# Performance work log

Measured on AMD Instinct MI355X. Metric: run time of the kernel, lower is better.

## Reference

```python
import jax, jax.numpy as jnp
import numpy as np

# ---- constants derived from init_kwargs ----
DETECT_THRESHOLD = 3.0
DETECT_SIGN = -1          # negative spikes
MARGIN_LEFT = 20          # snippet_T1
MARGIN_RIGHT = 20         # snippet_T2
CHANNEL_RADIUS = 100.0
SAMPLING_FREQUENCY = 30000.0
TIME_RADIUS = int(np.ceil(0.5 / 1000.0 * SAMPLING_FREQUENCY))  # = 15
MAX_DETECTIONS = 100000   # static cap for jit-compatible compaction


def setup_inputs() -> dict:
    key = jax.random.key(0)
    k1, k2 = jax.random.split(key)
    traces = jax.random.normal(k1, (150000, 384), dtype=jnp.float32)
    # spread channels over a 2000x2000 um area so radius=100 gives sparse adjacency
    channel_locations = jax.random.uniform(k2, (384, 2), dtype=jnp.float32) * 2000.0
    return {"traces": traces, "channel_locations": channel_locations}


def _detect_mask(traces, channel_locations):
    N, M = traces.shape
    # orientation (detect_sign < 0 -> traces_inv = -traces)
    if DETECT_SIGN > 0:
        traces_inv = traces
    elif DETECT_SIGN == 0:
        traces_inv = jnp.abs(traces)
    else:
        traces_inv = -traces

    # temporal max-pool, kernel 2*TR+1, stride 1, same padding (pads with -inf)
    pool = 2 * TIME_RADIUS + 1
    neg_inf = jnp.float32(-jnp.inf)
    temporal_max = jax.lax.reduce_window(
        traces_inv, neg_inf, jax.lax.max,
        window_dimensions=(pool, 1), window_strides=(1, 1),
        padding=((TIME_RADIUS, TIME_RADIUS), (0, 0)))  # [N, M]

    # channel adjacency from pairwise distances
    diff = channel_locations[:, None, :] - channel_locations[None, :, :]
    dists = jnp.sqrt(jnp.sum(diff * diff, axis=-1))  # [M, M]
    adj = dists <= CHANNEL_RADIUS

    # per-channel masked neighbor max over temporal_max columns -> [N, M]
    # sequential lax.map over channels avoids an N x M x M intermediate
    spatial_max = jax.lax.map(
        lambda row: jnp.max(jnp.where(row[None, :], temporal_max, neg_inf), axis=1),
        adj).T  # [N, M]

    t = jnp.arange(N)
    margin_ok = (t >= MARGIN_LEFT) & (t < N - MARGIN_RIGHT)  # [N]

    valid = ((traces_inv == temporal_max)
             & (traces_inv >= DETECT_THRESHOLD)
             & margin_ok[:, None]
             & (traces_inv >= spatial_max))
    return valid, traces_inv


def reference(traces, channel_locations):
    valid, _ = _detect_mask(traces, channel_locations)
    # row-major nonzero order == stable sort by time (row index)
    times, chans = jnp.nonzero(valid, size=MAX_DETECTIONS, fill_value=-1)
    return times.astype(jnp.int64), chans.astype(jnp.int32)
```

## Files before the change

### kernel.cpp

```cpp
#include <hip/hip_runtime.h>
#include <stdint.h>

#define M_CH       384
#define TR         15
#define MARGIN     20
#define CHUNK_ROWS 16
#define BM_WORDS   192
#define WPR        12
#define WIN_ROWS   46

__device__ __forceinline__ uint32_t spread4(uint32_t x) {
    x = (x | (x << 12)) & 0x000F000Fu;
    x = (x | (x << 6))  & 0x03030303u;
    x = (x | (x << 3))  & 0x11111111u;
    return x;
}

__global__ __launch_bounds__(256)
void cand_kernel(const float* __restrict__ traces,
                 const float* __restrict__ locs,
                 long n4, long nwords, int nbrBlock,
                 uint32_t* __restrict__ candWords,
                 uint32_t* __restrict__ nEntries,
                 uint8_t* __restrict__ entryWord,
                 uint32_t* __restrict__ entryMask) {
    if ((int)blockIdx.x >= nbrBlock) {
        __shared__ float lx[M_CH], ly[M_CH];
        const int t = threadIdx.x;
        for (int c = t; c < M_CH; c += 256) {
            lx[c] = locs[2 * c];
            ly[c] = locs[2 * c + 1];
        }
        __syncthreads();
        for (int c0 = t; c0 < M_CH; c0 += 256) {
            float x = lx[c0], y = ly[c0];
            int ne = 0;
            for (int k = 0; k < WPR; ++k) {
                uint32_t mk = 0;
                #pragma unroll
                for (int b = 0; b < 32; ++b) {
                    int c = k * 32 + b;
                    float dx = x - lx[c], dy = y - ly[c];
                    if (sqrtf(dx * dx + dy * dy) <= 100.0f) mk |= 1u << b;
                }
                if (mk) {
                    entryWord[c0 * WPR + ne] = (uint8_t)k;
                    entryMask[c0 * WPR + ne] = mk;
                    ne++;
                }
            }
            nEntries[c0] = (uint32_t)ne;
        }
        return;
    }

    const int lane = threadIdx.x & 63;
    const long wv = (((long)blockIdx.x * 256) + threadIdx.x) >> 6;
    const long fb = wv * 256;
    uint64_t B00,B01,B02,B03, B10,B11,B12,B13,
             B20,B21,B22,B23, B30,B31,B32,B33;
    {
        float4 v0 = make_float4(0,0,0,0), v1 = v0, v2 = v0, v3 = v0;
        long i0 = fb + 0 * 64 + lane;
        long i1 = fb + 1 * 64 + lane;
        long i2 = fb + 2 * 64 + lane;
        long i3 = fb + 3 * 64 + lane;
        if (i0 < n4) v0 = ((const float4*)traces)[i0];
        if (i1 < n4) v1 = ((const float4*)traces)[i1];
        if (i2 < n4) v2 = ((const float4*)traces)[i2];
        if (i3 < n4) v3 = ((const float4*)traces)[i3];
        B00 = __ballot(v0.x <= -3.0f); B01 = __ballot(v0.y <= -3.0f);
        B02 = __ballot(v0.z <= -3.0f); B03 = __ballot(v0.w <= -3.0f);
        B10 = __ballot(v1.x <= -3.0f); B11 = __ballot(v1.y <= -3.0f);
        B12 = __ballot(v1.z <= -3.0f); B13 = __ballot(v1.w <= -3.0f);
        B20 = __ballot(v2.x <= -3.0f); B21 = __ballot(v2.y <= -3.0f);
        B22 = __ballot(v2.z <= -3.0f); B23 = __ballot(v2.w <= -3.0f);
        B30 = __ballot(v3.x <= -3.0f); B31 = __ballot(v3.y <= -3.0f);
        B32 = __ballot(v3.z <= -3.0f); B33 = __ballot(v3.w <= -3.0f);
    }
    if (lane < 32) {
        int k  = lane >> 3;
        int sh = (lane & 7) * 8;
        uint64_t b0 = (k & 2) ? ((k & 1) ? B30 : B20) : ((k & 1) ? B10 : B00);
        uint64_t b1 = (k & 2) ? ((k & 1) ? B31 : B21) : ((k & 1) ? B11 : B01);
        uint64_t b2 = (k & 2) ? ((k & 1) ? B32 : B22) : ((k & 1) ? B12 : B02);
        uint64_t b3 = (k & 2) ? ((k & 1) ? B33 : B23) : ((k & 1) ? B13 : B03);
        uint32_t w = spread4((uint32_t)(b0 >> sh) & 0xFFu)
                   | (spread4((uint32_t)(b1 >> sh) & 0xFFu) << 1)
                   | (spread4((uint32_t)(b2 >> sh) & 0xFFu) << 2)
                   | (spread4((uint32_t)(b3 >> sh) & 0xFFu) << 3);
        long wIdx = wv * 32 + lane;
        if (wIdx < nwords) candWords[wIdx] = w;
    }
}

__global__ __launch_bounds__(192)
void validate_count_kernel(const float* __restrict__ traces, int N, long nwords,
                           const uint32_t* __restrict__ nEntries,
                           const uint8_t* __restrict__ entryWord,
                           const uint32_t* __restrict__ entryMask,
                           const uint32_t* __restrict__ candWords,
                           uint32_t* __restrict__ validOut,
                           uint32_t* __restrict__ chunkCounts) {
    __shared__ uint32_t win[WIN_ROWS * WPR];
    __shared__ uint32_t red[3];
    const int t = threadIdx.x;
    const int r0 = (int)blockIdx.x * CHUNK_ROWS;

    {
        const long base = (long)(r0 - TR) * WPR;
        #pragma unroll
        for (int i0 = 0; i0 < WIN_ROWS * WPR; i0 += 192) {
            int i = i0 + t;
            if (i < WIN_ROWS * WPR) {
                long g = base + i;
                win[i] = (g >= 0 && g < nwords) ? candWords[g] : 0u;
            }
        }
    }
    __syncthreads();

    const int lr = t / WPR;
    const int wi = t - lr * WPR;
    const int r  = r0 + lr;
    const long w = (long)blockIdx.x * BM_WORDS + t;

    uint32_t out = 0;
    if (w < nwords) {
        uint32_t word = win[(lr + TR) * WPR + wi];
        if (word && r >= MARGIN && r < N - MARGIN) {
            out = word;
            uint32_t tmp = word;
            while (tmp) {
                int bit = __ffs(tmp) - 1;
                tmp &= tmp - 1;
                const int c = wi * 32 + bit;
                const uint32_t selfbit = 1u << bit;
                const int ne = (int)nEntries[c];

                uint32_t anyComp = 0;
                for (int k = 0; k < ne; ++k) {
                    int wiE = (int)entryWord[c * WPR + k];
                    uint32_t em = entryMask[c * WPR + k];
                    const uint32_t* colp = &win[lr * WPR + wiE];
                    uint32_t orw = 0;
                    #pragma unroll
                    for (int dt = 0; dt < 31; ++dt) {
                        uint32_t h = colp[dt * WPR];
                        if (dt == TR) h &= (wiE == wi) ? ~selfbit : 0xFFFFFFFFu;
                        orw |= h & em;
                    }
                    anyComp |= orw;
                }

                if (anyComp) {
                    float raw = traces[(long)r * M_CH + c];
                    bool bad = false;
                    for (int k = 0; k < ne && !bad; ++k) {
                        int wiE = (int)entryWord[c * WPR + k];
                        uint32_t em = entryMask[c * WPR + k];
                        const uint32_t* colp = &win[lr * WPR + wiE];
                        #pragma unroll
                        for (int dt = 0; dt < 31; ++dt) {
                            uint32_t h = colp[dt * WPR] & em;
                            if (dt == TR && wiE == wi) h &= ~selfbit;
                            while (h) {
                                int b2 = __ffs(h) - 1;
                                h &= h - 1;
                                float v = traces[(long)(r - TR + dt) * M_CH + wiE * 32 + b2];
                                if (v < raw) bad = true;
                            }
                        }
                    }
                    if (bad) out &= ~selfbit;
                }
            }
        }
        validOut[w] = out;
    }
    int pc = __popc(out);
    #pragma unroll
    for (int off = 32; off; off >>= 1) pc += __shfl_xor(pc, off, 64);
    if ((t & 63) == 0) red[t >> 6] = (uint32_t)pc;
    __syncthreads();
    if (t == 0) chunkCounts[blockIdx.x] = red[0] + red[1] + red[2];
}

__global__ void scan_kernel(const uint32_t* __restrict__ counts, int n,
                            uint32_t* __restrict__ prefix) {
    __shared__ uint32_t s[256];
    int t = threadIdx.x;
    int per = (n + 255) / 256;
    int lo = t * per, hi = min(lo + per, n);
    uint32_t sum = 0;
    for (int i = lo; i < hi; ++i) sum += counts[i];
    s[t] = sum;
    __syncthreads();
    for (int off = 1; off < 256; off <<= 1) {
        uint32_t v = (t >= off) ? s[t - off] : 0;
        __syncthreads();
        s[t] += v;
        __syncthreads();
    }
    uint32_t run = s[t] - sum;
    for (int i = lo; i < hi; ++i) { prefix[i] = run; run += counts[i]; }
    if (t == 255) prefix[n] = run;
}

__global__ void emit_fill_kernel(const uint32_t* __restrict__ validOut,
                                 const uint32_t* __restrict__ chunkPrefix,
                                 int nchunk, int emitBlocks, int maxdet,
                                 int* __restrict__ times, int* __restrict__ chans) {
    if ((int)blockIdx.x >= emitBlocks) {
        int i = ((int)blockIdx.x - emitBlocks) * 256 + threadIdx.x;
        int total = (int)chunkPrefix[nchunk];
        if (i < maxdet && i >= total) { times[i] = -1; chans[i] = -1; }
        return;
    }
    int wv = threadIdx.x >> 6;
    int lane = threadIdx.x & 63;
    int chunkId = blockIdx.x * 4 + wv;
    if (chunkId >= nchunk) return;

    const uint32_t* wp = validOut + (long)chunkId * BM_WORDS + lane * 3;
    uint32_t b0 = wp[0], b1 = wp[1], b2 = wp[2];
    int local = __popc(b0) + __popc(b1) + __popc(b2);

    int s = local;
    #pragma unroll
    for (int off = 1; off < 64; off <<= 1) {
        int v = __shfl_up(s, off, 64);
        if (lane >= off) s += v;
    }
    int base = (int)chunkPrefix[chunkId] + (s - local);
    int r0 = chunkId * CHUNK_ROWS;

    uint32_t words[3] = { b0, b1, b2 };
    #pragma unroll
    for (int q = 0; q < 3; ++q) {
        uint32_t x = words[q];
        int fbase = (lane * 3 + q) * 32;
        while (x) {
            int b = __ffs(x) - 1;
            x &= x - 1;
            int f = fbase + b;
            int n = f / M_CH;
            int ch = f - n * M_CH;
            if (base < maxdet) {
                times[base] = r0 + n;
                chans[base] = ch;
            }
            base++;
        }
    }
}

extern "C" void kernel_launch(void* const* d_in, const int* in_sizes, int n_in,
                              void* d_out, int out_size, void* d_ws, size_t ws_size,
                              hipStream_t stream) {
    const float* traces = (const float*)d_in[0];
    const float* locs   = (const float*)d_in[1];
    const int M = M_CH;
    const int N = in_sizes[0] / M;
    const long nsamp = (long)N * M;
    const int maxdet = out_size / 2;
    int* times = (int*)d_out;
    int* chans = times + maxdet;

    const long n4     = nsamp / 4;
    const long nwords = nsamp / 32;
    const int  nchunk = (N + CHUNK_ROWS - 1) / CHUNK_ROWS;

    char* ws = (char*)d_ws;
    uint32_t* nEntries    = (uint32_t*)(ws + 0);
    uint8_t*  entryWord   = (uint8_t*)(ws + 1536);
    uint32_t* entryMask   = (uint32_t*)(ws + 6144);
    uint32_t* chunkCounts = (uint32_t*)(ws + 24576);
    uint32_t* chunkPrefix = (uint32_t*)(ws + 62080);
    uint32_t* candWords   = (uint32_t*)(ws + 99584);
    uint32_t* validOut    = (uint32_t*)(ws + 7299584);

    const long nwaves = (nwords + 31) / 32;
    const int  cblocks = (int)((nwaves + 3) / 4);
    cand_kernel<<<cblocks + 1, 256, 0, stream>>>(
        traces, locs, n4, nwords, cblocks,
        candWords, nEntries, entryWord, entryMask);

    validate_count_kernel<<<nchunk, BM_WORDS, 0, stream>>>(
        traces, N, nwords, nEntries, entryWord, entryMask, candWords,
        validOut, chunkCounts);

    scan_kernel<<<1, 256, 0, stream>>>(chunkCounts, nchunk, chunkPrefix);

    const int emitBlocks = (nchunk + 3) / 4;
    const int fillBlocks = (maxdet + 255) / 256;
    emit_fill_kernel<<<emitBlocks + fillBlocks, 256, 0, stream>>>(
        validOut, chunkPrefix, nchunk, emitBlocks, maxdet, times, chans);
}
```

Baseline: 449.3 us.

## Fuse validate, scan and emit into one kernel with decoupled look-back scan

```diff
diff --git a/kernel.cpp b/kernel.cpp
--- a/kernel.cpp
+++ b/kernel.cpp
@@ -9,6 +9,10 @@
 #define WPR        12
 #define WIN_ROWS   46
 
+#define VMASK  0x3FFFFFFFu
+#define AGG_F  (1u << 30)
+#define INCL_F (1u << 31)
+
 __device__ __forceinline__ uint32_t spread4(uint32_t x) {
     x = (x | (x << 12)) & 0x000F000Fu;
     x = (x | (x << 6))  & 0x03030303u;
@@ -23,8 +27,16 @@
                  uint32_t* __restrict__ candWords,
                  uint32_t* __restrict__ nEntries,
                  uint8_t* __restrict__ entryWord,
-                 uint32_t* __restrict__ entryMask) {
-    if ((int)blockIdx.x >= nbrBlock) {
+                 uint32_t* __restrict__ entryMask,
+                 uint32_t* __restrict__ status, int nStat,
+                 int maxdet, int* __restrict__ times, int* __restrict__ chans) {
+    if ((int)blockIdx.x > nbrBlock) {
+        int i = ((int)blockIdx.x - nbrBlock - 1) * 256 + threadIdx.x;
+        if (i < maxdet) { times[i] = -1; chans[i] = -1; }
+        if (i < nStat)  status[i] = 0u;
+        return;
+    }
+    if ((int)blockIdx.x == nbrBlock) {
         __shared__ float lx[M_CH], ly[M_CH];
         const int t = threadIdx.x;
         for (int c = t; c < M_CH; c += 256) {
@@ -95,25 +107,27 @@
 }
 
 __global__ __launch_bounds__(192)
-void validate_count_kernel(const float* __restrict__ traces, int N, long nwords,
-                           const uint32_t* __restrict__ nEntries,
-                           const uint8_t* __restrict__ entryWord,
-                           const uint32_t* __restrict__ entryMask,
-                           const uint32_t* __restrict__ candWords,
-                           uint32_t* __restrict__ validOut,
-                           uint32_t* __restrict__ chunkCounts) {
+void fused_kernel(const float* __restrict__ traces, int N, long nwords,
+                  const uint32_t* __restrict__ nEntries,
+                  const uint8_t* __restrict__ entryWord,
+                  const uint32_t* __restrict__ entryMask,
+                  const uint32_t* __restrict__ candWords,
+                  uint32_t* __restrict__ status,
+                  int maxdet, int* __restrict__ times, int* __restrict__ chans) {
     __shared__ uint32_t win[WIN_ROWS * WPR];
-    __shared__ uint32_t red[3];
+    __shared__ uint32_t wtot[3];
+    __shared__ uint32_t exclSh;
     const int t = threadIdx.x;
-    const int r0 = (int)blockIdx.x * CHUNK_ROWS;
+    const int bid = (int)blockIdx.x;
+    const int r0 = bid * CHUNK_ROWS;
 
     {
-        const long base = (long)(r0 - TR) * WPR;
+        const long gbase = (long)(r0 - TR) * WPR;
         #pragma unroll
         for (int i0 = 0; i0 < WIN_ROWS * WPR; i0 += 192) {
             int i = i0 + t;
             if (i < WIN_ROWS * WPR) {
-                long g = base + i;
+                long g = gbase + i;
                 win[i] = (g >= 0 && g < nwords) ? candWords[g] : 0u;
             }
         }
@@ -123,7 +137,7 @@
     const int lr = t / WPR;
     const int wi = t - lr * WPR;
     const int r  = r0 + lr;
-    const long w = (long)blockIdx.x * BM_WORDS + t;
+    const long w = (long)bid * BM_WORDS + t;
 
     uint32_t out = 0;
     if (w < nwords) {
@@ -176,82 +190,77 @@
                 }
             }
         }
-        validOut[w] = out;
-    }
+    }
+
+    const int lane = t & 63;
+    const int wvi  = t >> 6;
     int pc = __popc(out);
-    #pragma unroll
-    for (int off = 32; off; off >>= 1) pc += __shfl_xor(pc, off, 64);
-    if ((t & 63) == 0) red[t >> 6] = (uint32_t)pc;
-    __syncthreads();
-    if (t == 0) chunkCounts[blockIdx.x] = red[0] + red[1] + red[2];
-}
-
-__global__ void scan_kernel(const uint32_t* __restrict__ counts, int n,
-                            uint32_t* __restrict__ prefix) {
-    __shared__ uint32_t s[256];
-    int t = threadIdx.x;
-    int per = (n + 255) / 256;
-    int lo = t * per, hi = min(lo + per, n);
-    uint32_t sum = 0;
-    for (int i = lo; i < hi; ++i) sum += counts[i];
-    s[t] = sum;
-    __syncthreads();
-    for (int off = 1; off < 256; off <<= 1) {
-        uint32_t v = (t >= off) ? s[t - off] : 0;
-        __syncthreads();
-        s[t] += v;
-        __syncthreads();
-    }
-    uint32_t run = s[t] - sum;
-    for (int i = lo; i < hi; ++i) { prefix[i] = run; run += counts[i]; }
-    if (t == 255) prefix[n] = run;
-}
-
-__global__ void emit_fill_kernel(const uint32_t* __restrict__ validOut,
-                                 const uint32_t* __restrict__ chunkPrefix,
-                                 int nchunk, int emitBlocks, int maxdet,
-                                 int* __restrict__ times, int* __restrict__ chans) {
-    if ((int)blockIdx.x >= emitBlocks) {
-        int i = ((int)blockIdx.x - emitBlocks) * 256 + threadIdx.x;
-        int total = (int)chunkPrefix[nchunk];
-        if (i < maxdet && i >= total) { times[i] = -1; chans[i] = -1; }
-        return;
-    }
-    int wv = threadIdx.x >> 6;
-    int lane = threadIdx.x & 63;
-    int chunkId = blockIdx.x * 4 + wv;
-    if (chunkId >= nchunk) return;
-
-    const uint32_t* wp = validOut + (long)chunkId * BM_WORDS + lane * 3;
-    uint32_t b0 = wp[0], b1 = wp[1], b2 = wp[2];
-    int local = __popc(b0) + __popc(b1) + __popc(b2);
-
-    int s = local;
+    int s = pc;
     #pragma unroll
     for (int off = 1; off < 64; off <<= 1) {
         int v = __shfl_up(s, off, 64);
         if (lane >= off) s += v;
     }
-    int base = (int)chunkPrefix[chunkId] + (s - local);
-    int r0 = chunkId * CHUNK_ROWS;
-
-    uint32_t words[3] = { b0, b1, b2 };
-    #pragma unroll
-    for (int q = 0; q < 3; ++q) {
-        uint32_t x = words[q];
-        int fbase = (lane * 3 + q) * 32;
-        while (x) {
-            int b = __ffs(x) - 1;
-            x &= x - 1;
-            int f = fbase + b;
-            int n = f / M_CH;
-            int ch = f - n * M_CH;
-            if (base < maxdet) {
-                times[base] = r0 + n;
-                chans[base] = ch;
+    if (lane == 63) wtot[wvi] = (uint32_t)s;
+    __syncthreads();
+    const uint32_t cnt = wtot[0] + wtot[1] + wtot[2];
+
+    if (wvi == 0) {
+        if (lane == 0) atomicExch(&status[bid], AGG_F | cnt);
+        uint32_t running = 0;
+        if (bid > 0) {
+            long jw = bid - 1;
+            for (;;) {
+                int j = (int)(jw - lane);
+                uint32_t v = 0;
+                const bool valid = (j >= 0);
+                if (valid) {
+                    for (;;) {
+                        v = atomicOr(&status[j], 0u);
+                        if (v & (AGG_F | INCL_F)) break;
+                        __builtin_amdgcn_s_sleep(1);
+                    }
+                }
+                unsigned long long im = __ballot(valid && (v & INCL_F));
+                if (im) {
+                    int fi = __ffsll((long long)im) - 1;
+                    uint32_t contrib = (lane <= fi && valid) ? (v & VMASK) : 0u;
+                    #pragma unroll
+                    for (int off = 32; off; off >>= 1)
+                        contrib += __shfl_xor(contrib, off, 64);
+                    running += contrib;
+                    break;
+                } else {
+                    uint32_t contrib = valid ? (v & VMASK) : 0u;
+                    #pragma unroll
+                    for (int off = 32; off; off >>= 1)
+                        contrib += __shfl_xor(contrib, off, 64);
+                    running += contrib;
+                    jw -= 64;
+                    if (jw < 0) break;
+                }
             }
-            base++;
-        }
+        }
+        if (lane == 0) {
+            atomicExch(&status[bid], INCL_F | ((running + cnt) & VMASK));
+            exclSh = running;
+        }
+    }
+    __syncthreads();
+
+    const uint32_t excl = exclSh;
+    int woff = (wvi == 0) ? 0 : ((wvi == 1) ? (int)wtot[0]
+                                            : (int)(wtot[0] + wtot[1]));
+    int base = (int)excl + woff + (s - pc);
+    uint32_t x = out;
+    while (x) {
+        int b = __ffs(x) - 1;
+        x &= x - 1;
+        if (base < maxdet) {
+            times[base] = r;
+            chans[base] = wi * 32 + b;
+        }
+        base++;
     }
 }
 
@@ -270,30 +279,24 @@
     const long n4     = nsamp / 4;
     const long nwords = nsamp / 32;
     const int  nchunk = (N + CHUNK_ROWS - 1) / CHUNK_ROWS;
+    const int  nStat  = nchunk + 1;
 
     char* ws = (char*)d_ws;
     uint32_t* nEntries    = (uint32_t*)(ws + 0);
     uint8_t*  entryWord   = (uint8_t*)(ws + 1536);
     uint32_t* entryMask   = (uint32_t*)(ws + 6144);
-    uint32_t* chunkCounts = (uint32_t*)(ws + 24576);
-    uint32_t* chunkPrefix = (uint32_t*)(ws + 62080);
-    uint32_t* candWords   = (uint32_t*)(ws + 99584);
-    uint32_t* validOut    = (uint32_t*)(ws + 7299584);
+    uint32_t* status      = (uint32_t*)(ws + 24576);
+    uint32_t* candWords   = (uint32_t*)(ws + 65536);
 
     const long nwaves = (nwords + 31) / 32;
     const int  cblocks = (int)((nwaves + 3) / 4);
-    cand_kernel<<<cblocks + 1, 256, 0, stream>>>(
+    const int  fillBlocks = (maxdet + 255) / 256;
+    cand_kernel<<<cblocks + 1 + fillBlocks, 256, 0, stream>>>(
         traces, locs, n4, nwords, cblocks,
-        candWords, nEntries, entryWord, entryMask);
-
-    validate_count_kernel<<<nchunk, BM_WORDS, 0, stream>>>(
+        candWords, nEntries, entryWord, entryMask,
+        status, nStat, maxdet, times, chans);
+
+    fused_kernel<<<nchunk, BM_WORDS, 0, stream>>>(
         traces, N, nwords, nEntries, entryWord, entryMask, candWords,
-        validOut, chunkCounts);
-
-    scan_kernel<<<1, 256, 0, stream>>>(chunkCounts, nchunk, chunkPrefix);
-
-    const int emitBlocks = (nchunk + 3) / 4;
-    const int fillBlocks = (maxdet + 255) / 256;
-    emit_fill_kernel<<<emitBlocks + fillBlocks, 256, 0, stream>>>(
-        validOut, chunkPrefix, nchunk, emitBlocks, maxdet, times, chans);
+        status, maxdet, times, chans);
 }
```

Result: slower. 565.8 us (+25.9%).

## Drop scan kernel; emit blocks compute own prefix, move fill into cand kernel

Applied to the files above, without the earlier changes.

```diff
diff --git a/kernel.cpp b/kernel.cpp
--- a/kernel.cpp
+++ b/kernel.cpp
@@ -23,8 +23,14 @@
                  uint32_t* __restrict__ candWords,
                  uint32_t* __restrict__ nEntries,
                  uint8_t* __restrict__ entryWord,
-                 uint32_t* __restrict__ entryMask) {
-    if ((int)blockIdx.x >= nbrBlock) {
+                 uint32_t* __restrict__ entryMask,
+                 int maxdet, int* __restrict__ times, int* __restrict__ chans) {
+    if ((int)blockIdx.x > nbrBlock) {
+        int i = ((int)blockIdx.x - nbrBlock - 1) * 256 + threadIdx.x;
+        if (i < maxdet) { times[i] = -1; chans[i] = -1; }
+        return;
+    }
+    if ((int)blockIdx.x == nbrBlock) {
         __shared__ float lx[M_CH], ly[M_CH];
         const int t = threadIdx.x;
         for (int c = t; c < M_CH; c += 256) {
@@ -108,12 +114,12 @@
     const int r0 = (int)blockIdx.x * CHUNK_ROWS;
 
     {
-        const long base = (long)(r0 - TR) * WPR;
+        const long gbase = (long)(r0 - TR) * WPR;
         #pragma unroll
         for (int i0 = 0; i0 < WIN_ROWS * WPR; i0 += 192) {
             int i = i0 + t;
             if (i < WIN_ROWS * WPR) {
-                long g = base + i;
+                long g = gbase + i;
                 win[i] = (g >= 0 && g < nwords) ? candWords[g] : 0u;
             }
         }
@@ -186,41 +192,33 @@
     if (t == 0) chunkCounts[blockIdx.x] = red[0] + red[1] + red[2];
 }
 
-__global__ void scan_kernel(const uint32_t* __restrict__ counts, int n,
-                            uint32_t* __restrict__ prefix) {
-    __shared__ uint32_t s[256];
-    int t = threadIdx.x;
-    int per = (n + 255) / 256;
-    int lo = t * per, hi = min(lo + per, n);
-    uint32_t sum = 0;
-    for (int i = lo; i < hi; ++i) sum += counts[i];
-    s[t] = sum;
+__global__ __launch_bounds__(256)
+void emit_kernel(const uint32_t* __restrict__ validOut,
+                 const uint32_t* __restrict__ chunkCounts,
+                 int nchunk, int maxdet,
+                 int* __restrict__ times, int* __restrict__ chans) {
+    __shared__ uint32_t sred[4];
+    __shared__ uint32_t cnts4[4];
+    const int t = threadIdx.x;
+    const int lane = t & 63;
+    const int wv   = t >> 6;
+    const int c0 = (int)blockIdx.x * 4;
+
+    if (t < 4) cnts4[t] = (c0 + t < nchunk) ? chunkCounts[c0 + t] : 0u;
+
+    uint32_t part = 0;
+    for (int i = t; i < c0; i += 256) part += chunkCounts[i];
+    #pragma unroll
+    for (int off = 32; off; off >>= 1) part += __shfl_xor(part, off, 64);
+    if (lane == 0) sred[wv] = part;
     __syncthreads();
-    for (int off = 1; off < 256; off <<= 1) {
-        uint32_t v = (t >= off) ? s[t - off] : 0;
-        __syncthreads();
-        s[t] += v;
-        __syncthreads();
-    }
-    uint32_t run = s[t] - sum;
-    for (int i = lo; i < hi; ++i) { prefix[i] = run; run += counts[i]; }
-    if (t == 255) prefix[n] = run;
-}
-
-__global__ void emit_fill_kernel(const uint32_t* __restrict__ validOut,
-                                 const uint32_t* __restrict__ chunkPrefix,
-                                 int nchunk, int emitBlocks, int maxdet,
-                                 int* __restrict__ times, int* __restrict__ chans) {
-    if ((int)blockIdx.x >= emitBlocks) {
-        int i = ((int)blockIdx.x - emitBlocks) * 256 + threadIdx.x;
-        int total = (int)chunkPrefix[nchunk];
-        if (i < maxdet && i >= total) { times[i] = -1; chans[i] = -1; }
-        return;
-    }
-    int wv = threadIdx.x >> 6;
-    int lane = threadIdx.x & 63;
-    int chunkId = blockIdx.x * 4 + wv;
+    uint32_t base0 = sred[0] + sred[1] + sred[2] + sred[3];
+
+    const int chunkId = c0 + wv;
     if (chunkId >= nchunk) return;
+    uint32_t basePref = base0;
+    #pragma unroll
+    for (int k = 0; k < 3; ++k) if (k < wv) basePref += cnts4[k];
 
     const uint32_t* wp = validOut + (long)chunkId * BM_WORDS + lane * 3;
     uint32_t b0 = wp[0], b1 = wp[1], b2 = wp[2];
@@ -232,7 +230,7 @@
         int v = __shfl_up(s, off, 64);
         if (lane >= off) s += v;
     }
-    int base = (int)chunkPrefix[chunkId] + (s - local);
+    int base = (int)basePref + (s - local);
     int r0 = chunkId * CHUNK_ROWS;
 
     uint32_t words[3] = { b0, b1, b2 };
@@ -276,24 +274,22 @@
     uint8_t*  entryWord   = (uint8_t*)(ws + 1536);
     uint32_t* entryMask   = (uint32_t*)(ws + 6144);
     uint32_t* chunkCounts = (uint32_t*)(ws + 24576);
-    uint32_t* chunkPrefix = (uint32_t*)(ws + 62080);
-    uint32_t* candWords   = (uint32_t*)(ws + 99584);
-    uint32_t* validOut    = (uint32_t*)(ws + 7299584);
+    uint32_t* candWords   = (uint32_t*)(ws + 65536);
+    uint32_t* validOut    = (uint32_t*)(ws + 7265536);
 
     const long nwaves = (nwords + 31) / 32;
     const int  cblocks = (int)((nwaves + 3) / 4);
-    cand_kernel<<<cblocks + 1, 256, 0, stream>>>(
+    const int  fillBlocks = (maxdet + 255) / 256;
+    cand_kernel<<<cblocks + 1 + fillBlocks, 256, 0, stream>>>(
         traces, locs, n4, nwords, cblocks,
-        candWords, nEntries, entryWord, entryMask);
+        candWords, nEntries, entryWord, entryMask,
+        maxdet, times, chans);
 
     validate_count_kernel<<<nchunk, BM_WORDS, 0, stream>>>(
         traces, N, nwords, nEntries, entryWord, entryMask, candWords,
         validOut, chunkCounts);
 
-    scan_kernel<<<1, 256, 0, stream>>>(chunkCounts, nchunk, chunkPrefix);
-
     const int emitBlocks = (nchunk + 3) / 4;
-    const int fillBlocks = (maxdet + 255) / 256;
-    emit_fill_kernel<<<emitBlocks + fillBlocks, 256, 0, stream>>>(
-        validOut, chunkPrefix, nchunk, emitBlocks, maxdet, times, chans);
-}
+    emit_kernel<<<emitBlocks, 256, 0, stream>>>(
+        validOut, chunkCounts, nchunk, maxdet, times, chans);
+}
```

Result: faster. 437.5 us (-2.6%).
